# Kernel tuning notes

Hardware: AMD Instinct MI355X
Metric: run time of the kernel (lower is better)

The kernel has to match this reference:

```python
import jax, jax.numpy as jnp
import numpy as np

N = 20000   # nodes
IN = 128    # in_feats
H = 2       # n_heads
D = 32      # per-head dim (hid_feats = H*D = 64)
K = 3       # diffusion hops in AGDNConv
R = 5       # relations into dst type 'drug'
E = 320000  # edges per relation
NEG_SLOPE = 0.2


def setup_inputs() -> dict:
    key = jax.random.key(0)
    ks = jax.random.split(key, 11)
    s = 1.0 / np.sqrt(IN)
    return dict(
        h=jax.random.normal(ks[0], (N, IN), jnp.float32),
        src_idx=jax.random.randint(ks[1], (R, E), 0, N, dtype=jnp.int32),
        dst_idx=jax.random.randint(ks[2], (R, E), 0, N, dtype=jnp.int32),
        fc_w=jax.random.normal(ks[3], (R, IN, H * D), jnp.float32) * s,
        res_w=jax.random.normal(ks[4], (R, IN, H * D), jnp.float32) * s,
        attn_l=jax.random.normal(ks[5], (R, H, D), jnp.float32) * 0.1,
        attn_r=jax.random.normal(ks[6], (R, H, D), jnp.float32) * 0.1,
        hop_attn_l=jax.random.normal(ks[7], (R, H, D), jnp.float32) * 0.1,
        hop_attn_r=jax.random.normal(ks[8], (R, H, D), jnp.float32) * 0.1,
        w_rel=jax.random.normal(ks[9], (R, R), jnp.float32) * (1.0 / np.sqrt(R)),
        b_rel=jax.random.normal(ks[10], (R,), jnp.float32) * 0.1,
    )


def _agdn_conv(h, src, dst, fc_w, res_w, al, ar, hal, har):
    """One AGDNConv (GAT attention + K-hop diffusion + HA hop attention + residual)."""
    x = (h @ fc_w).reshape(N, H, D)                       # [N,H,D] projected feats
    el = jnp.sum(x * al, -1)                              # [N,H]
    er = jnp.sum(x * ar, -1)                              # [N,H]
    e = jax.nn.leaky_relu(el[src] + er[dst], NEG_SLOPE)   # [E,H] edge logits
    # segment softmax over incoming edges per dst node
    emax = jax.ops.segment_max(e, dst, num_segments=N)
    emax = jnp.where(jnp.isfinite(emax), emax, 0.0)
    ee = jnp.exp(e - emax[dst])
    denom = jax.ops.segment_sum(ee, dst, num_segments=N)
    alpha = ee / jnp.maximum(denom[dst], 1e-9)            # [E,H]

    def hop(hk, _):
        msg = alpha[:, :, None] * hk[src]                 # [E,H,D] gather+weight
        hk1 = jax.ops.segment_sum(msg, dst, num_segments=N)
        return hk1, hk1

    _, hks = jax.lax.scan(hop, x, None, length=K)         # [K,N,H,D]
    hops = jnp.concatenate([x[None], hks], axis=0)        # [K+1,N,H,D]
    # hop_norm: L2 normalize each hop's features
    hops = hops / jnp.maximum(jnp.linalg.norm(hops, axis=-1, keepdims=True), 1e-9)
    # HA hop attention
    hl = jnp.sum(hops * hal, -1)                          # [K+1,N,H]
    hr = jnp.sum(hops[0] * har, -1)                       # [N,H]
    hop_w = jax.nn.softmax(jax.nn.leaky_relu(hl + hr[None], NEG_SLOPE), axis=0)
    out = jnp.einsum('knh,knhd->nhd', hop_w, hops)        # [N,H,D]
    return out + (h @ res_w).reshape(N, H, D)             # residual


def reference(h, src_idx, dst_idx, fc_w, res_w, attn_l, attn_r, hop_attn_l, hop_attn_r, w_rel, b_rel):
    # per-relation AGDN convolutions (HeteroGraphConv dispatch)
    outs = jax.vmap(_agdn_conv, in_axes=(None, 0, 0, 0, 0, 0, 0, 0, 0))(
        h, src_idx, dst_idx, fc_w, res_w, attn_l, attn_r, hop_attn_l, hop_attn_r)  # [R,N,H,D]
    # my_agg_func2: learned relation weights = model_drug(ones(R))
    weights = w_rel @ jnp.ones((R,), jnp.float32) + b_rel  # [R]
    combined = jnp.einsum('r,rnhd->nhd', weights, outs)    # weighted relation sum
    return jnp.mean(combined, axis=1)                      # combine='mean' over heads -> [N,D]
```

## Files before the change

### kernel.cpp

```cpp
#include <hip/hip_runtime.h>
#include <hip/hip_bf16.h>

#define NN 20000
#define IN 128
#define HH 2
#define DD 32
#define HD 64
#define KK 3
#define RR 5
#define EE 320000
#define NEG 0.2f

#define PADK 136
#define NB 313
#define NBLK 64
#define CHUNK 5000
#define CAP 2048
#define NBCAP (NB * CAP)
#define RPS 20004
#define HTOT (NN * IN / 4)
#define PARTB (RR * NBLK)

typedef short v8s __attribute__((ext_vector_type(8)));
typedef float v4f __attribute__((ext_vector_type(4)));
typedef _Float16 hf8 __attribute__((ext_vector_type(8)));

__device__ __forceinline__ ushort f2b(float f) {
    unsigned u = __float_as_uint(f);
    unsigned r = (u + 0x7fff + ((u >> 16) & 1)) >> 16;
    return (ushort)r;
}
__device__ __forceinline__ ushort f2h(float f) {
    _Float16 h = (_Float16)f;
    return __builtin_bit_cast(ushort, h);
}
__device__ __forceinline__ float h2f(ushort u) {
    _Float16 h = __builtin_bit_cast(_Float16, u);
    return (float)h;
}
__device__ __forceinline__ float2 up2(unsigned u) {
    return make_float2(h2f((ushort)(u & 0xFFFF)), h2f((ushort)(u >> 16)));
}

__global__ __launch_bounds__(256) void cvt_kernel(
    const float* __restrict__ h, const float* __restrict__ fcw,
    const float* __restrict__ resw, ushort* __restrict__ wb,
    ushort* __restrict__ hb, int* __restrict__ bcnt)
{
    int j = blockIdx.x * 256 + threadIdx.x;
    if (j < RR * NB) bcnt[j] = 0;
    if (j < RR * 128 * IN) {
        int k = j & 127;
        int c = (j >> 7) & 127;
        int r = j >> 14;
        float v = (c < HD) ? fcw[(r * IN + k) * HD + c] : resw[(r * IN + k) * HD + (c - HD)];
        wb[j] = f2b(v);
    }
    int t = j - RR * 128 * IN;
    if (t >= 0 && t < HTOT) {
        float4 v = ((const float4*)h)[t];
        ((ushort4*)hb)[t] = make_ushort4(f2b(v.x), f2b(v.y), f2b(v.z), f2b(v.w));
    }
}

__global__ __launch_bounds__(256) void projpart_kernel(
    const ushort* __restrict__ hb, const ushort* __restrict__ wb,
    const float* __restrict__ attn_l, const float* __restrict__ attn_r,
    ushort* __restrict__ t0, ushort* __restrict__ resh,
    float* __restrict__ el, float* __restrict__ er,
    const int* __restrict__ src, const int* __restrict__ dst,
    int* __restrict__ bcnt, unsigned* __restrict__ bucketRec)
{
    __shared__ ushort As[64 * PADK];
    __shared__ ushort Bs[128 * PADK];
    int tid = threadIdx.x;

    if (blockIdx.x < PARTB) {
        int* hh = (int*)As;
        int r = blockIdx.x >> 6;
        int blk = blockIdx.x & 63;
        for (int i = tid; i < NB; i += 256) hh[i] = 0;
        __syncthreads();
        const int* S = src + (size_t)r * EE + blk * CHUNK;
        const int* D = dst + (size_t)r * EE + blk * CHUNK;
        for (int i = tid; i < CHUNK; i += 256)
            atomicAdd(&hh[D[i] >> 6], 1);
        __syncthreads();
        for (int i = tid; i < NB; i += 256) {
            int c = hh[i];
            hh[i] = c ? atomicAdd(&bcnt[r * NB + i], c) : 0;
        }
        __syncthreads();
        unsigned* BR = bucketRec + (size_t)r * NBCAP;
        for (int i = tid; i < CHUNK; i += 256) {
            int s = S[i], d = D[i];
            int b = d >> 6;
            int pos = atomicAdd(&hh[b], 1);
            if (pos < CAP)
                BR[((size_t)b << 11) + pos] = (unsigned)s | ((unsigned)(d & 63) << 15);
        }
        return;
    }

    int bx = blockIdx.x - PARTB;
    int r = bx / 313;
    int tile = bx - r * 313;
    int n0 = tile * 64;

    #pragma unroll
    for (int i = 0; i < 4; i++) {
        int c = tid + 256 * i;
        int row = c >> 4;
        int off = (c & 15) * 8;
        int gn = n0 + row;
        uint4 v = make_uint4(0u, 0u, 0u, 0u);
        if (gn < NN) v = *(const uint4*)&hb[(size_t)gn * IN + off];
        *(uint4*)&As[row * PADK + off] = v;
    }
    const ushort* wr = wb + (size_t)r * 128 * IN;
    #pragma unroll
    for (int i = 0; i < 8; i++) {
        int c = tid + 256 * i;
        int row = c >> 4;
        int off = (c & 15) * 8;
        *(uint4*)&Bs[row * PADK + off] = *(const uint4*)&wr[row * IN + off];
    }
    __syncthreads();

    int w = tid >> 6, lane = tid & 63;
    int lm = lane & 15, lq = lane >> 4;

    v4f acc[4][2];
    #pragma unroll
    for (int mt = 0; mt < 4; mt++)
        #pragma unroll
        for (int nt = 0; nt < 2; nt++) acc[mt][nt] = (v4f){0.f, 0.f, 0.f, 0.f};

    const ushort* Ab = &As[lm * PADK + lq * 8];
    const ushort* Bb = &Bs[(w * 32 + lm) * PADK + lq * 8];

    #pragma unroll
    for (int ks = 0; ks < 4; ks++) {
        v8s a[4], b[2];
        #pragma unroll
        for (int mt = 0; mt < 4; mt++) a[mt] = *(const v8s*)(Ab + mt * 16 * PADK + ks * 32);
        #pragma unroll
        for (int nt = 0; nt < 2; nt++) b[nt] = *(const v8s*)(Bb + nt * 16 * PADK + ks * 32);
        #pragma unroll
        for (int mt = 0; mt < 4; mt++)
            #pragma unroll
            for (int nt = 0; nt < 2; nt++)
                acc[mt][nt] = __builtin_amdgcn_mfma_f32_16x16x32_bf16(a[mt], b[nt], acc[mt][nt], 0, 0, 0);
    }

    int colbase = w * 32 + lm;
    #pragma unroll
    for (int mt = 0; mt < 4; mt++) {
        #pragma unroll
        for (int nt = 0; nt < 2; nt++) {
            int col = colbase + nt * 16;
            #pragma unroll
            for (int p = 0; p < 4; p++) {
                int node = n0 + mt * 16 + lq * 4 + p;
                if (node < NN) {
                    float v = acc[mt][nt][p];
                    if (col < HD) {
                        t0[((size_t)r * NN + node) * HD + col] = f2h(v);
                    } else {
                        resh[((size_t)r * NN + node) * HD + (col - HD)] = f2h(v);
                    }
                }
            }
        }
    }

    if (w < 2) {
        float al0 = attn_l[(r * HH + w) * DD + lm];
        float al1 = attn_l[(r * HH + w) * DD + lm + 16];
        float ar0 = attn_r[(r * HH + w) * DD + lm];
        float ar1 = attn_r[(r * HH + w) * DD + lm + 16];
        #pragma unroll
        for (int mt = 0; mt < 4; mt++) {
            #pragma unroll
            for (int p = 0; p < 4; p++) {
                float pl = acc[mt][0][p] * al0 + acc[mt][1][p] * al1;
                float pr = acc[mt][0][p] * ar0 + acc[mt][1][p] * ar1;
                #pragma unroll
                for (int off = 1; off < 16; off <<= 1) {
                    pl += __shfl_xor(pl, off, 64);
                    pr += __shfl_xor(pr, off, 64);
                }
                if (lm == 0) {
                    int node = n0 + mt * 16 + lq * 4 + p;
                    if (node < NN) {
                        el[((size_t)r * NN + node) * HH + w] = pl;
                        er[((size_t)r * NN + node) * HH + w] = pr;
                    }
                }
            }
        }
    }
}

__global__ __launch_bounds__(256) void bsort_alpha_hop1_kernel(
    const unsigned* __restrict__ bucketRec, const int* __restrict__ bcnt,
    const float* __restrict__ el, const float* __restrict__ er,
    const ushort* __restrict__ t0, uint2* __restrict__ csrE,
    int* __restrict__ rowp, ushort* __restrict__ t1)
{
    __shared__ int cnt64s[4][64];
    __shared__ int segS[65];
    __shared__ int cur[64];
    __shared__ int pbS[64];
    __shared__ float2 erL[64];
    __shared__ float2 mx2[64];
    __shared__ float2 inv2[64];
    __shared__ unsigned sSD[CAP];
    __shared__ unsigned sL[CAP];

    int bk = blockIdx.x;
    int r = bk / NB;
    int bkt = bk - r * NB;
    int tid = threadIdx.x;
    int wv = tid >> 6;
    int cnt = bcnt[bk];
    if (cnt > CAP - 64) cnt = CAP - 64;

    if (tid < 64) {
        cnt64s[0][tid] = 0; cnt64s[1][tid] = 0;
        cnt64s[2][tid] = 0; cnt64s[3][tid] = 0;
        int gn = bkt * 64 + tid;
        erL[tid] = (gn < NN) ? ((const float2*)er)[(size_t)r * NN + gn]
                             : make_float2(0.f, 0.f);
    }
    __syncthreads();
    const unsigned* BR = bucketRec + (size_t)bk * CAP;
    for (int i = tid; i < cnt; i += 256)
        atomicAdd(&cnt64s[wv][(BR[i] >> 15) & 63], 1);
    __syncthreads();
    if (tid < 64) {
        int v = cnt64s[0][tid] + cnt64s[1][tid] + cnt64s[2][tid] + cnt64s[3][tid];
        int x = v;
        int y = v & 1;
        #pragma unroll
        for (int off = 1; off < 64; off <<= 1) {
            int tx = __shfl_up(x, off, 64);
            int ty = __shfl_up(y, off, 64);
            if (tid >= off) { x += tx; y += ty; }
        }
        segS[tid] = x - v;
        cur[tid]  = x - v;
        pbS[tid]  = (x - v) + (y - (v & 1));
        if (tid == 63) segS[64] = x;
    }
    __syncthreads();
    const float2* el2 = (const float2*)el + (size_t)r * NN;
    for (int i = tid; i < cnt; i += 256) {
        unsigned rec = BR[i];
        int s = rec & 0x7FFF;
        int d = (rec >> 15) & 63;
        float2 a = el2[s];
        float2 b = erL[d];
        float l0 = a.x + b.x; l0 = l0 > 0.f ? l0 : NEG * l0;
        float l1 = a.y + b.y; l1 = l1 > 0.f ? l1 : NEG * l1;
        int pos = atomicAdd(&cur[d], 1);
        sSD[pos] = rec;
        sL[pos] = (unsigned)f2h(l0) | ((unsigned)f2h(l1) << 16);
    }
    __syncthreads();
    {
        int d = tid >> 2, sub = tid & 3;
        int b0 = segS[d], e0 = segS[d + 1];
        float m0 = -1e30f, m1 = -1e30f;
        for (int i = b0 + sub; i < e0; i += 4) {
            float2 l = up2(sL[i]);
            m0 = fmaxf(m0, l.x); m1 = fmaxf(m1, l.y);
        }
        m0 = fmaxf(m0, __shfl_xor(m0, 1, 64));
        m0 = fmaxf(m0, __shfl_xor(m0, 2, 64));
        m1 = fmaxf(m1, __shfl_xor(m1, 1, 64));
        m1 = fmaxf(m1, __shfl_xor(m1, 2, 64));
        float s0 = 0.f, s1 = 0.f;
        for (int i = b0 + sub; i < e0; i += 4) {
            float2 l = up2(sL[i]);
            s0 += __expf(l.x - m0); s1 += __expf(l.y - m1);
        }
        s0 += __shfl_xor(s0, 1, 64); s0 += __shfl_xor(s0, 2, 64);
        s1 += __shfl_xor(s1, 1, 64); s1 += __shfl_xor(s1, 2, 64);
        if (sub == 0) {
            mx2[d] = make_float2(m0, m1);
            inv2[d] = make_float2(1.f / fmaxf(s0, 1e-9f), 1.f / fmaxf(s1, 1e-9f));
            int gn = bkt * 64 + d;
            if (gn < NN) {
                int len = e0 - b0;
                rowp[r * RPS + gn] =
                    (int)(((unsigned)(bkt * CAP + pbS[d])) | ((unsigned)len << 20));
            }
        }
    }
    __syncthreads();
    uint2* E = csrE + (size_t)bk * CAP;
    for (int i = tid; i < cnt; i += 256) {
        unsigned rec = sSD[i];
        int d = (rec >> 15) & 63;
        float2 l = up2(sL[i]);
        float w0 = __expf(l.x - mx2[d].x) * inv2[d].x;
        float w1 = __expf(l.y - mx2[d].y) * inv2[d].y;
        unsigned wp = (unsigned)f2h(w0) | ((unsigned)f2h(w1) << 16);
        E[pbS[d] + (i - segS[d])] = make_uint2(rec, wp);
        sL[i] = wp;
    }
    if (tid < 64) {
        int len = segS[tid + 1] - segS[tid];
        if (len & 1) E[pbS[tid] + len] = make_uint2(0u, 0u);
    }
    __syncthreads();

    int lane = tid & 63;
    int g = lane >> 3;
    int f = (lane & 7) * 8;
    int sh = ((lane >> 2) & 1) * 16;
    const ushort* T0 = t0 + (size_t)r * NN * HD;
    #pragma unroll
    for (int half = 0; half < 2; half++) {
        int d = half * 32 + wv * 8 + g;
        int b0 = segS[d];
        int len = segS[d + 1] - b0;
        float acc[8] = {0.f, 0.f, 0.f, 0.f, 0.f, 0.f, 0.f, 0.f};
        if (len > 0) {
            float wC = h2f((ushort)(sL[b0] >> sh));
            int sC = sSD[b0] & 0x7FFF;
            hf8 fC = *(const hf8*)&T0[(size_t)sC * HD + f];
            for (int j = 0; j < len; j++) {
                int jn = j + 1 < len ? j + 1 : len - 1;
                float wN = h2f((ushort)(sL[b0 + jn] >> sh));
                int sN = sSD[b0 + jn] & 0x7FFF;
                hf8 fN = *(const hf8*)&T0[(size_t)sN * HD + f];
                #pragma unroll
                for (int k = 0; k < 8; k++) acc[k] += wC * (float)fC[k];
                wC = wN; fC = fN;
            }
        }
        int node = bkt * 64 + d;
        if (node < NN) {
            ushort o[8];
            #pragma unroll
            for (int k = 0; k < 8; k++) o[k] = f2h(acc[k]);
            *(uint4*)&t1[((size_t)r * NN + node) * HD + f] = *(uint4*)o;
        }
    }
}

__global__ __launch_bounds__(256) void hop_kernel(
    const ushort* __restrict__ tin, ushort* __restrict__ tout,
    const uint2* __restrict__ csrE, const int* __restrict__ rowp)
{
    int nbk = gridDim.x;
    int q = nbk >> 3, rmd = nbk & 7;
    int xcd = blockIdx.x & 7, pos = blockIdx.x >> 3;
    int bid = (xcd < rmd ? xcd * (q + 1) : rmd * (q + 1) + (xcd - rmd) * q) + pos;

    int w = (bid * 256 + (int)threadIdx.x) >> 6;
    if (w >= RR * (NN / 8)) return;
    int lane = threadIdx.x & 63;
    int g = lane >> 3;
    int f = (lane & 7) * 8;
    int sh = ((lane >> 2) & 1) * 16;
    int r = w / (NN / 8);
    int n0 = (w - r * (NN / 8)) * 8;

    unsigned pv = (unsigned)rowp[r * RPS + n0 + g];
    int bg = (int)(pv & 0xFFFFF);
    int len = (int)(pv >> 20);
    int pairs = (len + 1) >> 1;
    int lastP = pairs > 0 ? pairs - 1 : 0;

    const ushort* T = tin + (size_t)r * NN * HD;
    const uint4* E4 = (const uint4*)(csrE + (size_t)r * NBCAP);
    int base4 = bg >> 1;

    uint4 rC = E4[base4];
    uint4 rN = E4[base4 + (1 < pairs ? 1 : lastP)];
    int s0 = (int)(rC.x & 0x7FFF); s0 = s0 < NN ? s0 : 0;
    int s1 = (int)(rC.z & 0x7FFF); s1 = s1 < NN ? s1 : 0;
    hf8 f0 = *(const hf8*)&T[(size_t)s0 * HD + f];
    hf8 f1 = *(const hf8*)&T[(size_t)s1 * HD + f];

    float acc[8] = {0.f, 0.f, 0.f, 0.f, 0.f, 0.f, 0.f, 0.f};
    #pragma unroll 2
    for (int j = 0; j < pairs; j++) {
        int j2 = j + 2 < pairs ? j + 2 : lastP;
        uint4 r2 = E4[base4 + j2];
        int n0i = (int)(rN.x & 0x7FFF); n0i = n0i < NN ? n0i : 0;
        int n1i = (int)(rN.z & 0x7FFF); n1i = n1i < NN ? n1i : 0;
        hf8 g0 = *(const hf8*)&T[(size_t)n0i * HD + f];
        hf8 g1 = *(const hf8*)&T[(size_t)n1i * HD + f];
        float w0 = h2f((ushort)(rC.y >> sh));
        float w1 = h2f((ushort)(rC.w >> sh));
        #pragma unroll
        for (int k = 0; k < 8; k++) {
            acc[k] += w0 * (float)f0[k];
            acc[k] += w1 * (float)f1[k];
        }
        rC = rN; rN = r2;
        f0 = g0; f1 = g1;
    }
    ushort o[8];
    #pragma unroll
    for (int k = 0; k < 8; k++) o[k] = f2h(acc[k]);
    *(uint4*)&tout[((size_t)r * NN + n0 + g) * HD + f] = *(uint4*)o;
}

__global__ __launch_bounds__(256) void final_kernel(
    const ushort* __restrict__ t0, const ushort* __restrict__ t1,
    const ushort* __restrict__ t2, const ushort* __restrict__ t3,
    const ushort* __restrict__ resh,
    const float* __restrict__ hal, const float* __restrict__ har,
    const float* __restrict__ w_rel, const float* __restrict__ b_rel,
    float* __restrict__ out)
{
    int idx = blockIdx.x * 256 + threadIdx.x;
    if (idx >= NN * HH * 4) return;
    int fq = idx & 3;
    int h_ = (idx >> 2) & 1;
    int n = idx >> 3;
    const ushort* tb[4] = {t0, t1, t2, t3};
    float o[8];
    #pragma unroll
    for (int d = 0; d < 8; d++) o[d] = 0.f;

    for (int r = 0; r < RR; r++) {
        float wr = b_rel[r];
        #pragma unroll
        for (int j = 0; j < RR; j++) wr += w_rel[r * RR + j];
        const float* hp = hal + (r * HH + h_) * DD + fq * 8;
        const float* gp = har + (r * HH + h_) * DD + fq * 8;
        float4 ha0 = *(const float4*)hp;
        float4 ha1 = *(const float4*)(hp + 4);
        float4 hr0 = *(const float4*)gp;
        float4 hr1 = *(const float4*)(gp + 4);
        float halc[8] = {ha0.x, ha0.y, ha0.z, ha0.w, ha1.x, ha1.y, ha1.z, ha1.w};
        float harc[8] = {hr0.x, hr0.y, hr0.z, hr0.w, hr1.x, hr1.y, hr1.z, hr1.w};

        size_t tbase = ((size_t)r * NN + n) * HD + h_ * DD + fq * 8;
        uint4 tv[4];
        float sq[4], dl[4], dr = 0.f;
        #pragma unroll
        for (int k = 0; k < 4; k++) {
            tv[k] = *(const uint4*)(tb[k] + tbase);
            unsigned ww[4] = {tv[k].x, tv[k].y, tv[k].z, tv[k].w};
            float s = 0.f, d1 = 0.f;
            #pragma unroll
            for (int j = 0; j < 4; j++) {
                float2 v = up2(ww[j]);
                s  += v.x * v.x + v.y * v.y;
                d1 += v.x * halc[2 * j] + v.y * halc[2 * j + 1];
                if (k == 0)
                    dr += v.x * harc[2 * j] + v.y * harc[2 * j + 1];
            }
            sq[k] = s; dl[k] = d1;
        }
        #pragma unroll
        for (int k = 0; k < 4; k++) {
            sq[k] += __shfl_xor(sq[k], 1, 64); sq[k] += __shfl_xor(sq[k], 2, 64);
            dl[k] += __shfl_xor(dl[k], 1, 64); dl[k] += __shfl_xor(dl[k], 2, 64);
        }
        dr += __shfl_xor(dr, 1, 64); dr += __shfl_xor(dr, 2, 64);

        float inv[4], lg[4], mx = -1e30f;
        #pragma unroll
        for (int k = 0; k < 4; k++)
            inv[k] = 1.f / fmaxf(sqrtf(sq[k]), 1e-9f);
        #pragma unroll
        for (int k = 0; k < 4; k++) {
            float l = dl[k] * inv[k] + dr * inv[0];
            l = l > 0.f ? l : NEG * l;
            lg[k] = l;
            mx = fmaxf(mx, l);
        }
        float ssum = 0.f;
        #pragma unroll
        for (int k = 0; k < 4; k++) { lg[k] = __expf(lg[k] - mx); ssum += lg[k]; }
        float sw = wr / ssum;
        #pragma unroll
        for (int k = 0; k < 4; k++) {
            float coef = lg[k] * inv[k] * sw;
            unsigned ww[4] = {tv[k].x, tv[k].y, tv[k].z, tv[k].w};
            #pragma unroll
            for (int j = 0; j < 4; j++) {
                float2 v = up2(ww[j]);
                o[2 * j]     += coef * v.x;
                o[2 * j + 1] += coef * v.y;
            }
        }
        uint4 rv = *(const uint4*)(resh + tbase);
        unsigned rw[4] = {rv.x, rv.y, rv.z, rv.w};
        #pragma unroll
        for (int j = 0; j < 4; j++) {
            float2 v = up2(rw[j]);
            o[2 * j]     += wr * v.x;
            o[2 * j + 1] += wr * v.y;
        }
    }
    float p[8];
    #pragma unroll
    for (int j = 0; j < 8; j++) p[j] = __shfl_down(o[j], 4, 64);
    if (h_ == 0) {
        float4* op = (float4*)(out + (size_t)n * DD + fq * 8);
        op[0] = make_float4(0.5f * (o[0] + p[0]), 0.5f * (o[1] + p[1]),
                            0.5f * (o[2] + p[2]), 0.5f * (o[3] + p[3]));
        op[1] = make_float4(0.5f * (o[4] + p[4]), 0.5f * (o[5] + p[5]),
                            0.5f * (o[6] + p[6]), 0.5f * (o[7] + p[7]));
    }
}

extern "C" void kernel_launch(void* const* d_in, const int* in_sizes, int n_in,
                              void* d_out, int out_size, void* d_ws, size_t ws_size,
                              hipStream_t stream) {
    (void)in_sizes; (void)n_in; (void)out_size; (void)ws_size;
    const float* h     = (const float*)d_in[0];
    const int*   src   = (const int*)d_in[1];
    const int*   dst   = (const int*)d_in[2];
    const float* fcw   = (const float*)d_in[3];
    const float* resw  = (const float*)d_in[4];
    const float* atl   = (const float*)d_in[5];
    const float* atr   = (const float*)d_in[6];
    const float* hal   = (const float*)d_in[7];
    const float* har   = (const float*)d_in[8];
    const float* wrel  = (const float*)d_in[9];
    const float* brel  = (const float*)d_in[10];
    float* out = (float*)d_out;

    float* ws = (float*)d_ws;
    size_t off = 0;
    float* el   = ws + off;  off += (size_t)RR * NN * HH;
    float* er   = ws + off;  off += (size_t)RR * NN * HH;
    uint2* csrE = (uint2*)(ws + off);      off += (size_t)RR * NBCAP * 2;
    unsigned* bucketRec = (unsigned*)(ws + off); off += (size_t)RR * NBCAP;
    ushort* resh = (ushort*)(ws + off);    off += (size_t)RR * NN * HD / 2;
    ushort* t0  = (ushort*)(ws + off);     off += (size_t)RR * NN * HD / 2;
    ushort* t1  = (ushort*)(ws + off);     off += (size_t)RR * NN * HD / 2;
    ushort* t2  = (ushort*)(ws + off);     off += (size_t)RR * NN * HD / 2;
    ushort* t3  = (ushort*)(ws + off);     off += (size_t)RR * NN * HD / 2;
    ushort* wb  = (ushort*)(ws + off);     off += (size_t)RR * 128 * IN / 2;
    ushort* hb  = (ushort*)(ws + off);     off += (size_t)NN * IN / 2;
    int* rowp   = (int*)(ws + off);  off += (size_t)RR * RPS;
    int* bcnt   = (int*)(ws + off);  off += (size_t)RR * NB;

    cvt_kernel<<<(RR * 128 * IN + HTOT + 255) / 256, 256, 0, stream>>>(h, fcw, resw, wb, hb, bcnt);
    projpart_kernel<<<PARTB + 313 * RR, 256, 0, stream>>>(hb, wb, atl, atr, t0, resh, el, er,
                                                          src, dst, bcnt, bucketRec);
    bsort_alpha_hop1_kernel<<<RR * NB, 256, 0, stream>>>(bucketRec, bcnt, el, er, t0, csrE, rowp, t1);
    hop_kernel<<<(RR * (NN / 8) + 3) / 4, 256, 0, stream>>>(t1, t2, csrE, rowp);
    hop_kernel<<<(RR * (NN / 8) + 3) / 4, 256, 0, stream>>>(t2, t3, csrE, rowp);
    final_kernel<<<(NN * HH * 4 + 255) / 256, 256, 0, stream>>>(t0, t1, t2, t3, resh, hal, har, wrel, brel, out);
}
```

Baseline: 214.2 us.

## Fuse third hop into final combine and stage projection stores through LDS

The last diffusion hop is merged into the final hop-attention kernel. Each wave computes the hop-3 row in registers instead of writing and rereading t3, and the per-relation results are accumulated into the output with float atomics, which needs an output zeroing step added to the conversion kernel. The projection kernel now reads the weight tile straight from global memory rather than staging it in LDS, and it writes t0/resh through an LDS transpose so the stores are coalesced 16-byte writes. The atomics add contention on output rows and make the summation order nondeterministic.

```diff
diff --git a/kernel.cpp b/kernel.cpp
--- a/kernel.cpp
+++ b/kernel.cpp
@@ -45,10 +45,13 @@
 __global__ __launch_bounds__(256) void cvt_kernel(
     const float* __restrict__ h, const float* __restrict__ fcw,
     const float* __restrict__ resw, ushort* __restrict__ wb,
-    ushort* __restrict__ hb, int* __restrict__ bcnt)
+    ushort* __restrict__ hb, int* __restrict__ bcnt,
+    float* __restrict__ out)
 {
     int j = blockIdx.x * 256 + threadIdx.x;
     if (j < RR * NB) bcnt[j] = 0;
+    if (j < NN * DD / 4)
+        ((float4*)out)[j] = make_float4(0.f, 0.f, 0.f, 0.f);
     if (j < RR * 128 * IN) {
         int k = j & 127;
         int c = (j >> 7) & 127;
@@ -72,7 +75,6 @@
     int* __restrict__ bcnt, unsigned* __restrict__ bucketRec)
 {
     __shared__ ushort As[64 * PADK];
-    __shared__ ushort Bs[128 * PADK];
     int tid = threadIdx.x;
 
     if (blockIdx.x < PARTB) {
@@ -117,14 +119,6 @@
         if (gn < NN) v = *(const uint4*)&hb[(size_t)gn * IN + off];
         *(uint4*)&As[row * PADK + off] = v;
     }
-    const ushort* wr = wb + (size_t)r * 128 * IN;
-    #pragma unroll
-    for (int i = 0; i < 8; i++) {
-        int c = tid + 256 * i;
-        int row = c >> 4;
-        int off = (c & 15) * 8;
-        *(uint4*)&Bs[row * PADK + off] = *(const uint4*)&wr[row * IN + off];
-    }
     __syncthreads();
 
     int w = tid >> 6, lane = tid & 63;
@@ -137,7 +131,8 @@
         for (int nt = 0; nt < 2; nt++) acc[mt][nt] = (v4f){0.f, 0.f, 0.f, 0.f};
 
     const ushort* Ab = &As[lm * PADK + lq * 8];
-    const ushort* Bb = &Bs[(w * 32 + lm) * PADK + lq * 8];
+    const ushort* wr = wb + (size_t)r * 128 * IN;
+    const ushort* Bg = wr + (size_t)(w * 32 + lm) * IN + lq * 8;
 
     #pragma unroll
     for (int ks = 0; ks < 4; ks++) {
@@ -145,33 +140,12 @@
         #pragma unroll
         for (int mt = 0; mt < 4; mt++) a[mt] = *(const v8s*)(Ab + mt * 16 * PADK + ks * 32);
         #pragma unroll
-        for (int nt = 0; nt < 2; nt++) b[nt] = *(const v8s*)(Bb + nt * 16 * PADK + ks * 32);
+        for (int nt = 0; nt < 2; nt++) b[nt] = *(const v8s*)(Bg + nt * 16 * IN + ks * 32);
         #pragma unroll
         for (int mt = 0; mt < 4; mt++)
             #pragma unroll
             for (int nt = 0; nt < 2; nt++)
                 acc[mt][nt] = __builtin_amdgcn_mfma_f32_16x16x32_bf16(a[mt], b[nt], acc[mt][nt], 0, 0, 0);
-    }
-
-    int colbase = w * 32 + lm;
-    #pragma unroll
-    for (int mt = 0; mt < 4; mt++) {
-        #pragma unroll
-        for (int nt = 0; nt < 2; nt++) {
-            int col = colbase + nt * 16;
-            #pragma unroll
-            for (int p = 0; p < 4; p++) {
-                int node = n0 + mt * 16 + lq * 4 + p;
-                if (node < NN) {
-                    float v = acc[mt][nt][p];
-                    if (col < HD) {
-                        t0[((size_t)r * NN + node) * HD + col] = f2h(v);
-                    } else {
-                        resh[((size_t)r * NN + node) * HD + (col - HD)] = f2h(v);
-                    }
-                }
-            }
-        }
     }
 
     if (w < 2) {
@@ -200,6 +174,28 @@
             }
         }
     }
+
+    __syncthreads();
+    int colbase = w * 32 + lm;
+    #pragma unroll
+    for (int mt = 0; mt < 4; mt++)
+        #pragma unroll
+        for (int nt = 0; nt < 2; nt++)
+            #pragma unroll
+            for (int p = 0; p < 4; p++)
+                As[(mt * 16 + lq * 4 + p) * PADK + colbase + nt * 16] = f2h(acc[mt][nt][p]);
+    __syncthreads();
+    #pragma unroll
+    for (int i = 0; i < 2; i++) {
+        int c = tid + 256 * i;
+        int row = c >> 3;
+        int off = (c & 7) * 8;
+        int gn = n0 + row;
+        if (gn < NN) {
+            *(uint4*)&t0[((size_t)r * NN + gn) * HD + off]   = *(const uint4*)&As[row * PADK + off];
+            *(uint4*)&resh[((size_t)r * NN + gn) * HD + off] = *(const uint4*)&As[row * PADK + 64 + off];
+        }
+    }
 }
 
 __global__ __launch_bounds__(256) void bsort_alpha_hop1_kernel(
@@ -411,106 +407,167 @@
     *(uint4*)&tout[((size_t)r * NN + n0 + g) * HD + f] = *(uint4*)o;
 }
 
-__global__ __launch_bounds__(256) void final_kernel(
+__global__ __launch_bounds__(256) void hop3_final_kernel(
     const ushort* __restrict__ t0, const ushort* __restrict__ t1,
-    const ushort* __restrict__ t2, const ushort* __restrict__ t3,
-    const ushort* __restrict__ resh,
+    const ushort* __restrict__ t2, const ushort* __restrict__ resh,
+    const uint2* __restrict__ csrE, const int* __restrict__ rowp,
     const float* __restrict__ hal, const float* __restrict__ har,
     const float* __restrict__ w_rel, const float* __restrict__ b_rel,
     float* __restrict__ out)
 {
-    int idx = blockIdx.x * 256 + threadIdx.x;
-    if (idx >= NN * HH * 4) return;
-    int fq = idx & 3;
-    int h_ = (idx >> 2) & 1;
-    int n = idx >> 3;
-    const ushort* tb[4] = {t0, t1, t2, t3};
+    int nbk = gridDim.x;
+    int q = nbk >> 3, rmd = nbk & 7;
+    int xcd = blockIdx.x & 7, pos = blockIdx.x >> 3;
+    int bid = (xcd < rmd ? xcd * (q + 1) : rmd * (q + 1) + (xcd - rmd) * q) + pos;
+
+    int wid = (bid * 256 + (int)threadIdx.x) >> 6;
+    if (wid >= RR * (NN / 8)) return;
+    int lane = threadIdx.x & 63;
+    int g = lane >> 3;
+    int ll = lane & 7;
+    int f = ll * 8;
+    int h_ = ll >> 2;
+    int fq = ll & 3;
+    int sh = h_ * 16;
+    int r = wid / (NN / 8);
+    int n = (wid - r * (NN / 8)) * 8 + g;
+
+    unsigned pv = (unsigned)rowp[r * RPS + n];
+    int bg = (int)(pv & 0xFFFFF);
+    int len = (int)(pv >> 20);
+    int pairs = (len + 1) >> 1;
+    int lastP = pairs > 0 ? pairs - 1 : 0;
+
+    const ushort* T = t2 + (size_t)r * NN * HD;
+    const uint4* E4 = (const uint4*)(csrE + (size_t)r * NBCAP);
+    int base4 = bg >> 1;
+
+    uint4 rC = E4[base4];
+    uint4 rN = E4[base4 + (1 < pairs ? 1 : lastP)];
+    int s0 = (int)(rC.x & 0x7FFF); s0 = s0 < NN ? s0 : 0;
+    int s1 = (int)(rC.z & 0x7FFF); s1 = s1 < NN ? s1 : 0;
+    hf8 f0 = *(const hf8*)&T[(size_t)s0 * HD + f];
+    hf8 f1 = *(const hf8*)&T[(size_t)s1 * HD + f];
+
+    float t3row[8] = {0.f, 0.f, 0.f, 0.f, 0.f, 0.f, 0.f, 0.f};
+    #pragma unroll 2
+    for (int j = 0; j < pairs; j++) {
+        int j2 = j + 2 < pairs ? j + 2 : lastP;
+        uint4 r2 = E4[base4 + j2];
+        int n0i = (int)(rN.x & 0x7FFF); n0i = n0i < NN ? n0i : 0;
+        int n1i = (int)(rN.z & 0x7FFF); n1i = n1i < NN ? n1i : 0;
+        hf8 g0 = *(const hf8*)&T[(size_t)n0i * HD + f];
+        hf8 g1 = *(const hf8*)&T[(size_t)n1i * HD + f];
+        float w0 = h2f((ushort)(rC.y >> sh));
+        float w1 = h2f((ushort)(rC.w >> sh));
+        #pragma unroll
+        for (int k = 0; k < 8; k++) {
+            t3row[k] += w0 * (float)f0[k];
+            t3row[k] += w1 * (float)f1[k];
+        }
+        rC = rN; rN = r2;
+        f0 = g0; f1 = g1;
+    }
+
+    float wr = b_rel[r];
+    #pragma unroll
+    for (int j = 0; j < RR; j++) wr += w_rel[r * RR + j];
+    const float* hp = hal + (r * HH + h_) * DD + fq * 8;
+    const float* gp = har + (r * HH + h_) * DD + fq * 8;
+    float4 ha0 = *(const float4*)hp;
+    float4 ha1 = *(const float4*)(hp + 4);
+    float4 hr0 = *(const float4*)gp;
+    float4 hr1 = *(const float4*)(gp + 4);
+    float halc[8] = {ha0.x, ha0.y, ha0.z, ha0.w, ha1.x, ha1.y, ha1.z, ha1.w};
+    float harc[8] = {hr0.x, hr0.y, hr0.z, hr0.w, hr1.x, hr1.y, hr1.z, hr1.w};
+
+    size_t tbase = ((size_t)r * NN + n) * HD + f;
+    const ushort* tb[3] = {t0, t1, t2};
+    uint4 tv[3];
+    float sq[4], dl[4], dr = 0.f;
+    #pragma unroll
+    for (int k = 0; k < 3; k++) {
+        tv[k] = *(const uint4*)(tb[k] + tbase);
+        unsigned ww[4] = {tv[k].x, tv[k].y, tv[k].z, tv[k].w};
+        float s = 0.f, d1 = 0.f;
+        #pragma unroll
+        for (int j = 0; j < 4; j++) {
+            float2 v = up2(ww[j]);
+            s  += v.x * v.x + v.y * v.y;
+            d1 += v.x * halc[2 * j] + v.y * halc[2 * j + 1];
+            if (k == 0)
+                dr += v.x * harc[2 * j] + v.y * harc[2 * j + 1];
+        }
+        sq[k] = s; dl[k] = d1;
+    }
+    {
+        float s = 0.f, d1 = 0.f;
+        #pragma unroll
+        for (int j = 0; j < 8; j++) {
+            s += t3row[j] * t3row[j];
+            d1 += t3row[j] * halc[j];
+        }
+        sq[3] = s; dl[3] = d1;
+    }
+    #pragma unroll
+    for (int k = 0; k < 4; k++) {
+        sq[k] += __shfl_xor(sq[k], 1, 64); sq[k] += __shfl_xor(sq[k], 2, 64);
+        dl[k] += __shfl_xor(dl[k], 1, 64); dl[k] += __shfl_xor(dl[k], 2, 64);
+    }
+    dr += __shfl_xor(dr, 1, 64); dr += __shfl_xor(dr, 2, 64);
+
+    float inv[4], lg[4], mx = -1e30f;
+    #pragma unroll
+    for (int k = 0; k < 4; k++)
+        inv[k] = 1.f / fmaxf(sqrtf(sq[k]), 1e-9f);
+    #pragma unroll
+    for (int k = 0; k < 4; k++) {
+        float l = dl[k] * inv[k] + dr * inv[0];
+        l = l > 0.f ? l : NEG * l;
+        lg[k] = l;
+        mx = fmaxf(mx, l);
+    }
+    float ssum = 0.f;
+    #pragma unroll
+    for (int k = 0; k < 4; k++) { lg[k] = __expf(lg[k] - mx); ssum += lg[k]; }
+    float sw = wr / ssum;
+
     float o[8];
     #pragma unroll
     for (int d = 0; d < 8; d++) o[d] = 0.f;
-
-    for (int r = 0; r < RR; r++) {
-        float wr = b_rel[r];
-        #pragma unroll
-        for (int j = 0; j < RR; j++) wr += w_rel[r * RR + j];
-        const float* hp = hal + (r * HH + h_) * DD + fq * 8;
-        const float* gp = har + (r * HH + h_) * DD + fq * 8;
-        float4 ha0 = *(const float4*)hp;
-        float4 ha1 = *(const float4*)(hp + 4);
-        float4 hr0 = *(const float4*)gp;
-        float4 hr1 = *(const float4*)(gp + 4);
-        float halc[8] = {ha0.x, ha0.y, ha0.z, ha0.w, ha1.x, ha1.y, ha1.z, ha1.w};
-        float harc[8] = {hr0.x, hr0.y, hr0.z, hr0.w, hr1.x, hr1.y, hr1.z, hr1.w};
-
-        size_t tbase = ((size_t)r * NN + n) * HD + h_ * DD + fq * 8;
-        uint4 tv[4];
-        float sq[4], dl[4], dr = 0.f;
-        #pragma unroll
-        for (int k = 0; k < 4; k++) {
-            tv[k] = *(const uint4*)(tb[k] + tbase);
-            unsigned ww[4] = {tv[k].x, tv[k].y, tv[k].z, tv[k].w};
-            float s = 0.f, d1 = 0.f;
-            #pragma unroll
-            for (int j = 0; j < 4; j++) {
-                float2 v = up2(ww[j]);
-                s  += v.x * v.x + v.y * v.y;
-                d1 += v.x * halc[2 * j] + v.y * halc[2 * j + 1];
-                if (k == 0)
-                    dr += v.x * harc[2 * j] + v.y * harc[2 * j + 1];
-            }
-            sq[k] = s; dl[k] = d1;
-        }
-        #pragma unroll
-        for (int k = 0; k < 4; k++) {
-            sq[k] += __shfl_xor(sq[k], 1, 64); sq[k] += __shfl_xor(sq[k], 2, 64);
-            dl[k] += __shfl_xor(dl[k], 1, 64); dl[k] += __shfl_xor(dl[k], 2, 64);
-        }
-        dr += __shfl_xor(dr, 1, 64); dr += __shfl_xor(dr, 2, 64);
-
-        float inv[4], lg[4], mx = -1e30f;
-        #pragma unroll
-        for (int k = 0; k < 4; k++)
-            inv[k] = 1.f / fmaxf(sqrtf(sq[k]), 1e-9f);
-        #pragma unroll
-        for (int k = 0; k < 4; k++) {
-            float l = dl[k] * inv[k] + dr * inv[0];
-            l = l > 0.f ? l : NEG * l;
-            lg[k] = l;
-            mx = fmaxf(mx, l);
-        }
-        float ssum = 0.f;
-        #pragma unroll
-        for (int k = 0; k < 4; k++) { lg[k] = __expf(lg[k] - mx); ssum += lg[k]; }
-        float sw = wr / ssum;
-        #pragma unroll
-        for (int k = 0; k < 4; k++) {
-            float coef = lg[k] * inv[k] * sw;
-            unsigned ww[4] = {tv[k].x, tv[k].y, tv[k].z, tv[k].w};
-            #pragma unroll
-            for (int j = 0; j < 4; j++) {
-                float2 v = up2(ww[j]);
-                o[2 * j]     += coef * v.x;
-                o[2 * j + 1] += coef * v.y;
-            }
-        }
-        uint4 rv = *(const uint4*)(resh + tbase);
-        unsigned rw[4] = {rv.x, rv.y, rv.z, rv.w};
+    #pragma unroll
+    for (int k = 0; k < 3; k++) {
+        float coef = lg[k] * inv[k] * sw;
+        unsigned ww[4] = {tv[k].x, tv[k].y, tv[k].z, tv[k].w};
         #pragma unroll
         for (int j = 0; j < 4; j++) {
-            float2 v = up2(rw[j]);
-            o[2 * j]     += wr * v.x;
-            o[2 * j + 1] += wr * v.y;
-        }
-    }
+            float2 v = up2(ww[j]);
+            o[2 * j]     += coef * v.x;
+            o[2 * j + 1] += coef * v.y;
+        }
+    }
+    {
+        float coef = lg[3] * inv[3] * sw;
+        #pragma unroll
+        for (int j = 0; j < 8; j++) o[j] += coef * t3row[j];
+    }
+    uint4 rv = *(const uint4*)(resh + tbase);
+    unsigned rw[4] = {rv.x, rv.y, rv.z, rv.w};
+    #pragma unroll
+    for (int j = 0; j < 4; j++) {
+        float2 v = up2(rw[j]);
+        o[2 * j]     += wr * v.x;
+        o[2 * j + 1] += wr * v.y;
+    }
+
     float p[8];
     #pragma unroll
     for (int j = 0; j < 8; j++) p[j] = __shfl_down(o[j], 4, 64);
     if (h_ == 0) {
-        float4* op = (float4*)(out + (size_t)n * DD + fq * 8);
-        op[0] = make_float4(0.5f * (o[0] + p[0]), 0.5f * (o[1] + p[1]),
-                            0.5f * (o[2] + p[2]), 0.5f * (o[3] + p[3]));
-        op[1] = make_float4(0.5f * (o[4] + p[4]), 0.5f * (o[5] + p[5]),
-                            0.5f * (o[6] + p[6]), 0.5f * (o[7] + p[7]));
+        float* op = out + (size_t)n * DD + fq * 8;
+        #pragma unroll
+        for (int j = 0; j < 8; j++)
+            unsafeAtomicAdd(&op[j], 0.5f * (o[j] + p[j]));
     }
 }
 
@@ -541,17 +598,16 @@
     ushort* t0  = (ushort*)(ws + off);     off += (size_t)RR * NN * HD / 2;
     ushort* t1  = (ushort*)(ws + off);     off += (size_t)RR * NN * HD / 2;
     ushort* t2  = (ushort*)(ws + off);     off += (size_t)RR * NN * HD / 2;
-    ushort* t3  = (ushort*)(ws + off);     off += (size_t)RR * NN * HD / 2;
     ushort* wb  = (ushort*)(ws + off);     off += (size_t)RR * 128 * IN / 2;
     ushort* hb  = (ushort*)(ws + off);     off += (size_t)NN * IN / 2;
     int* rowp   = (int*)(ws + off);  off += (size_t)RR * RPS;
     int* bcnt   = (int*)(ws + off);  off += (size_t)RR * NB;
 
-    cvt_kernel<<<(RR * 128 * IN + HTOT + 255) / 256, 256, 0, stream>>>(h, fcw, resw, wb, hb, bcnt);
+    cvt_kernel<<<(RR * 128 * IN + HTOT + 255) / 256, 256, 0, stream>>>(h, fcw, resw, wb, hb, bcnt, out);
     projpart_kernel<<<PARTB + 313 * RR, 256, 0, stream>>>(hb, wb, atl, atr, t0, resh, el, er,
                                                           src, dst, bcnt, bucketRec);
     bsort_alpha_hop1_kernel<<<RR * NB, 256, 0, stream>>>(bucketRec, bcnt, el, er, t0, csrE, rowp, t1);
     hop_kernel<<<(RR * (NN / 8) + 3) / 4, 256, 0, stream>>>(t1, t2, csrE, rowp);
-    hop_kernel<<<(RR * (NN / 8) + 3) / 4, 256, 0, stream>>>(t2, t3, csrE, rowp);
-    final_kernel<<<(NN * HH * 4 + 255) / 256, 256, 0, stream>>>(t0, t1, t2, t3, resh, hal, har, wrel, brel, out);
-}
+    hop3_final_kernel<<<(RR * (NN / 8) + 3) / 4, 256, 0, stream>>>(t0, t1, t2, resh, csrE, rowp,
+                                                                   hal, har, wrel, brel, out);
+}
```

Measured after the change: 276.8 us. 29.2% more time.
